# Kernel tuning notes

Hardware: AMD Instinct MI355X
Metric: run time of the kernel (lower is better)

## Reference

```python
import jax, jax.numpy as jnp
import numpy as np

HEADS = 8
DIM_HEAD = 32
SCALE = DIM_HEAD ** -0.5


def _split_heads(t):
    # [b, n, h*d] -> [b, h, n, d]
    b, n, hd = t.shape
    return t.reshape(b, n, HEADS, hd // HEADS).transpose(0, 2, 1, 3)


def setup_inputs() -> dict:
    key = jax.random.key(0)
    k1, k2, k3, k4 = jax.random.split(key, 4)
    b, n, dim = 2, 2048, 256
    inner = HEADS * DIM_HEAD  # 256
    x = jax.random.normal(k1, (b, n, dim), dtype=jnp.float32)
    attn_feat = jax.random.normal(k2, (b, n, dim), dtype=jnp.float32)
    # nn.Linear(dim, 3*inner, bias=False): store as [dim, 3*inner] for x @ W
    W_qkv = jax.random.normal(k3, (dim, 3 * inner), dtype=jnp.float32) * (dim ** -0.5)
    W_qkv_aux = jax.random.normal(k4, (dim, 3 * inner), dtype=jnp.float32) * (dim ** -0.5)
    return {"x": x, "attn_feat": attn_feat, "W_qkv": W_qkv, "W_qkv_aux": W_qkv_aux,
            "use_cls_tokens": 1}


def reference(x, attn_feat, W_qkv, W_qkv_aux, use_cls_tokens):
    b, n, dim = x.shape
    # aux Q,K (v_aux computed but unused, matching original chunk of 3)
    qkv_aux = attn_feat @ W_qkv_aux            # [b, n, 3*inner]
    q_aux, k_aux, _ = jnp.split(qkv_aux, 3, axis=-1)
    q_aux, k_aux = _split_heads(q_aux), _split_heads(k_aux)
    # self Q,K
    qkv_self = x @ W_qkv
    q_self, k_self, _ = jnp.split(qkv_self, 3, axis=-1)
    q_self, k_self = _split_heads(q_self), _split_heads(k_self)
    # dual score product: (QK^T_aux * scale) * (QK^T_self * scale)
    dots_aux = jnp.einsum('bhid,bhjd->bhij', q_aux, k_aux) * SCALE
    dots_self = jnp.einsum('bhid,bhjd->bhij', q_self, k_self) * SCALE
    attn = jax.nn.softmax(dots_aux * dots_self, axis=-1)  # [b, h, n, n]
    # v = x.unsqueeze(1): broadcast raw x over heads
    out = jnp.einsum('bhij,bjd->bhid', attn, x)           # [b, h, n, dim]
    out = out.transpose(0, 2, 1, 3).reshape(b, n, HEADS * dim)
    attn_flat = attn.transpose(0, 2, 1, 3).reshape(b, n, HEADS * n)
    return (out, out[:, 0], attn_flat[:, 0])
```

## Files before the change

### kernel.cpp

```cpp
#include <hip/hip_runtime.h>

typedef _Float16 f16;
typedef _Float16 f16x4 __attribute__((ext_vector_type(4)));
typedef _Float16 f16x8 __attribute__((ext_vector_type(8)));
typedef float f32x4 __attribute__((ext_vector_type(4)));

#define LOG2E 1.4426950408889634f
#define SCL   (1.4426950408889634f / 32.0f)
#define TH_RAW 177.445f

__global__ __launch_bounds__(256) void k_W(const float* __restrict__ Wq,
    const float* __restrict__ Wa, f16* __restrict__ Wt) {
  __shared__ f16 tile[64][65];
  int n0 = blockIdx.x * 64, k0 = blockIdx.y * 64, s = blockIdx.z;
  const float* W = s ? Wa : Wq;
  f16* dst = Wt + (size_t)s * 512 * 256;
  int t = threadIdx.x, c = t & 63, rg = t >> 6;
#pragma unroll
  for (int r = 0; r < 16; ++r) {
    int krow = r * 4 + rg;
    tile[krow][c] = (f16)W[(size_t)(k0 + krow) * 768 + n0 + c];
  }
  __syncthreads();
#pragma unroll
  for (int r = 0; r < 16; ++r) {
    int nrow = r * 4 + rg;
    dst[(size_t)(n0 + nrow) * 256 + k0 + c] = tile[c][nrow];
  }
}

__global__ __launch_bounds__(256) void k_proj(const float* __restrict__ x,
    const float* __restrict__ af, const f16* __restrict__ Wt,
    f16* __restrict__ Qs, f16* __restrict__ Ks,
    f16* __restrict__ Qa, f16* __restrict__ Ka, f16* __restrict__ xt) {
  __shared__ f16 tile[64][65];
  int t = threadIdx.x;
  if (blockIdx.x >= 64) {
    int r = ((blockIdx.z * 8 + blockIdx.y) * 16 + (blockIdx.x - 64));
    int n0 = (r & 31) * 64, d0 = ((r >> 5) & 3) * 64, b = r >> 7;
    int c = t & 63, rg = t >> 6;
#pragma unroll
    for (int rr = 0; rr < 16; ++rr) {
      int row = rr * 4 + rg;
      tile[row][c] = (f16)x[((size_t)b * 2048 + n0 + row) * 256 + d0 + c];
    }
    __syncthreads();
#pragma unroll
    for (int rr = 0; rr < 16; ++rr) {
      int drow = rr * 4 + rg;
      xt[((size_t)b * 256 + d0 + drow) * 2048 + n0 + c] = tile[c][drow];
    }
    return;
  }
  int mt = blockIdx.x, nt = blockIdx.y, s = blockIdx.z;
  const float* A = s ? af : x;
  const f16* W = Wt + (size_t)s * 512 * 256;
  f16* Qd = s ? Qa : Qs;
  f16* Kd = s ? Ka : Ks;
  int wv = t >> 6, ln = t & 63, cl = ln & 15, g = ln >> 4;
  int m0 = mt * 64, n0 = nt * 64;
  const float* arow = A + (size_t)(m0 + wv * 16 + cl) * 256 + g * 8;
  const f16* wb = W + (size_t)n0 * 256 + g * 8;
  f32x4 z4 = {0.f, 0.f, 0.f, 0.f};
  f32x4 acc[4] = {z4, z4, z4, z4};
#pragma unroll
  for (int k32 = 0; k32 < 8; ++k32) {
    float4 u = *(const float4*)(arow + k32 * 32);
    float4 v = *(const float4*)(arow + k32 * 32 + 4);
    f16x8 a = { (f16)u.x, (f16)u.y, (f16)u.z, (f16)u.w,
                (f16)v.x, (f16)v.y, (f16)v.z, (f16)v.w };
#pragma unroll
    for (int n4 = 0; n4 < 4; ++n4) {
      f16x8 bf = *(const f16x8*)(wb + (size_t)(n4 * 16 + cl) * 256 + k32 * 32);
      acc[n4] = __builtin_amdgcn_mfma_f32_16x16x32_f16(a, bf, acc[n4], 0, 0, 0);
    }
  }
#pragma unroll
  for (int n4 = 0; n4 < 4; ++n4) {
    int c = n0 + n4 * 16 + cl;
    int head = (c & 255) >> 5, d = c & 31;
    f16* dst = (c < 256) ? Qd : Kd;
#pragma unroll
    for (int r = 0; r < 4; ++r) {
      int m = m0 + wv * 16 + g * 4 + r;
      int bb = m >> 11, nn = m & 2047;
      dst[(((size_t)bb * 8 + head) * 2048 + nn) * 32 + d] = (f16)acc[n4][r];
    }
  }
}

__global__ __launch_bounds__(256, 2) void k_flash(const f16* __restrict__ Qs,
    const f16* __restrict__ Ks, const f16* __restrict__ Qa,
    const f16* __restrict__ Ka, const f16* __restrict__ xt,
    float* __restrict__ out, float* __restrict__ out_cls,
    float* __restrict__ attn0) {
  __shared__ f16 KaL[2][64][40];
  __shared__ f16 KsL[2][64][40];
  __shared__ f16 PL[2][64][72];
  __shared__ float alphaL[2][64] __attribute__((aligned(16)));
  __shared__ int   rsF[2][4] __attribute__((aligned(16)));
  __shared__ float lL[64];
  __shared__ float mHist[32];
  __shared__ float mFinS;
  int qt = blockIdx.x, h = blockIdx.y, b = blockIdx.z;
  int bh = b * 8 + h;
  int t = threadIdx.x, wv = t >> 6, ln = t & 63, cl = ln & 15, g = ln >> 4;
  bool isA0 = (qt == 0) && (wv == 0);
  float* a0base = attn0 + (size_t)b * 16384 + h * 2048;
  int qrow0 = qt * 64 + wv * 16;
  f16x8 qsf = *(const f16x8*)&Qs[((size_t)bh * 2048 + qrow0 + cl) * 32 + g * 8];
  f16x8 qaf = *(const f16x8*)&Qa[((size_t)bh * 2048 + qrow0 + cl) * 32 + g * 8];
  f32x4 z4 = {0.f, 0.f, 0.f, 0.f};
  f32x4 acc[4][4];
#pragma unroll
  for (int i = 0; i < 4; ++i)
#pragma unroll
    for (int j = 0; j < 4; ++j) acc[i][j] = z4;
  float m_run = -3.0e38f, l_lane = 0.f;
  int krow = t >> 2, koff = (t & 3) * 8;
  const f16* kaSrc = Ka + ((size_t)bh * 2048 + krow) * 32 + koff;
  const f16* ksSrc = Ks + ((size_t)bh * 2048 + krow) * 32 + koff;
  const f16* xb = xt + ((size_t)b * 256 + wv * 64) * 2048;

  float tv[16];
  f16x8 xf[2][4];

  auto SCORE_MM = [&](int buf) {
#pragma unroll
    for (int jt = 0; jt < 4; ++jt) {
      f16x8 kaf = *(const f16x8*)&KaL[buf][jt * 16 + cl][g * 8];
      f16x8 ksf = *(const f16x8*)&KsL[buf][jt * 16 + cl][g * 8];
      f32x4 za = __builtin_amdgcn_mfma_f32_16x16x32_f16(kaf, qaf, z4, 0, 0, 0);
      f32x4 zs = __builtin_amdgcn_mfma_f32_16x16x32_f16(ksf, qsf, z4, 0, 0, 0);
#pragma unroll
      for (int r = 0; r < 4; ++r) tv[jt * 4 + r] = za[r] * zs[r];
    }
  };

  auto SCORE_FIN = [&](int buf, int kt) {
    float a0 = fmaxf(tv[0], tv[1]),   a1 = fmaxf(tv[2], tv[3]);
    float a2 = fmaxf(tv[4], tv[5]),   a3 = fmaxf(tv[6], tv[7]);
    float a4 = fmaxf(tv[8], tv[9]),   a5 = fmaxf(tv[10], tv[11]);
    float a6 = fmaxf(tv[12], tv[13]), a7 = fmaxf(tv[14], tv[15]);
    float b0 = fmaxf(a0, a1), b1 = fmaxf(a2, a3);
    float b2 = fmaxf(a4, a5), b3 = fmaxf(a6, a7);
    float lmax = fmaxf(fmaxf(b0, b1), fmaxf(b2, b3));
    int wflag = 0;
    if (__any(lmax > m_run + TH_RAW)) {
      float tm = fmaxf(lmax, __shfl_xor(lmax, 16, 64));
      tm = fmaxf(tm, __shfl_xor(tm, 32, 64));
      float m_new = fmaxf(m_run, tm);
      float alpha = exp2f((m_run - m_new) * SCL);
      l_lane *= alpha;
      m_run = m_new;
      if (g == 0) alphaL[buf][wv * 16 + cl] = alpha;
      wflag = 1;
    }
    float mS = m_run * SCL;
    float p[16];
#pragma unroll
    for (int i = 0; i < 16; ++i) p[i] = exp2f(fmaf(tv[i], SCL, -mS));
    float s0 = p[0] + p[1],   s1 = p[2] + p[3];
    float s2 = p[4] + p[5],   s3 = p[6] + p[7];
    float s4 = p[8] + p[9],   s5 = p[10] + p[11];
    float s6 = p[12] + p[13], s7 = p[14] + p[15];
    float u0 = s0 + s1, u1 = s2 + s3, u2 = s4 + s5, u3 = s6 + s7;
    l_lane += (u0 + u1) + (u2 + u3);
#pragma unroll
    for (int jt = 0; jt < 4; ++jt) {
      auto lo = __builtin_amdgcn_cvt_pkrtz(p[jt * 4 + 0], p[jt * 4 + 1]);
      auto hi = __builtin_amdgcn_cvt_pkrtz(p[jt * 4 + 2], p[jt * 4 + 3]);
      f16x4 pk = { (f16)lo[0], (f16)lo[1], (f16)hi[0], (f16)hi[1] };
      *(f16x4*)&PL[buf][wv * 16 + cl][jt * 16 + g * 4] = pk;
    }
    if (ln == 0) rsF[buf][wv] = wflag;
    if (isA0) {
      if (ln == 0) mHist[kt] = m_run;
      if (cl == 0) {
#pragma unroll
        for (int jt = 0; jt < 4; ++jt) {
          float4 pw = { p[jt * 4 + 0], p[jt * 4 + 1],
                        p[jt * 4 + 2], p[jt * 4 + 3] };
          *(float4*)(a0base + kt * 64 + jt * 16 + g * 4) = pw;
        }
      }
    }
  };

  auto XFLOAD = [&](int kt) {
#pragma unroll
    for (int ks2 = 0; ks2 < 2; ++ks2)
#pragma unroll
      for (int ddt = 0; ddt < 4; ++ddt)
        xf[ks2][ddt] = *(const f16x8*)(xb + (size_t)(ddt * 16 + cl) * 2048 +
                                       kt * 64 + ks2 * 32 + g * 8);
  };

  auto PVDO = [&](int pbuf) {
    int4 fl = *(const int4*)&rsF[pbuf][0];
    int flq[4] = { fl.x, fl.y, fl.z, fl.w };
#pragma unroll
    for (int qt2 = 0; qt2 < 4; ++qt2) {
      if (flq[qt2]) {
        f32x4 a4 = *(const f32x4*)&alphaL[pbuf][qt2 * 16 + g * 4];
#pragma unroll
        for (int ddt = 0; ddt < 4; ++ddt)
#pragma unroll
          for (int r = 0; r < 4; ++r) acc[qt2][ddt][r] *= a4[r];
      }
    }
#pragma unroll
    for (int ks2 = 0; ks2 < 2; ++ks2) {
      f16x8 pf[4];
#pragma unroll
      for (int qt2 = 0; qt2 < 4; ++qt2)
        pf[qt2] = *(const f16x8*)&PL[pbuf][qt2 * 16 + cl][ks2 * 32 + g * 8];
#pragma unroll
      for (int ddt = 0; ddt < 4; ++ddt)
#pragma unroll
        for (int qt2 = 0; qt2 < 4; ++qt2)
          acc[qt2][ddt] = __builtin_amdgcn_mfma_f32_16x16x32_f16(
              pf[qt2], xf[ks2][ddt], acc[qt2][ddt], 0, 0, 0);
    }
  };

  *(f16x8*)&KaL[0][krow][koff] = *(const f16x8*)kaSrc;
  *(f16x8*)&KsL[0][krow][koff] = *(const f16x8*)ksSrc;
  __syncthreads();

  f16x8 kan = *(const f16x8*)(kaSrc + 2048);
  f16x8 ksn = *(const f16x8*)(ksSrc + 2048);
  SCORE_MM(0);
  SCORE_FIN(0, 0);
  *(f16x8*)&KaL[1][krow][koff] = kan;
  *(f16x8*)&KsL[1][krow][koff] = ksn;
  __syncthreads();

  for (int k = 1; k < 32; ++k) {
    int sbuf = k & 1, pbuf = sbuf ^ 1;
    XFLOAD(k - 1);
    if (k < 31) {
      kan = *(const f16x8*)(kaSrc + (size_t)(k + 1) * 2048);
      ksn = *(const f16x8*)(ksSrc + (size_t)(k + 1) * 2048);
    }
    SCORE_MM(sbuf);
    PVDO(pbuf);
    SCORE_FIN(sbuf, k);
    if (k < 31) {
      *(f16x8*)&KaL[pbuf][krow][koff] = kan;
      *(f16x8*)&KsL[pbuf][krow][koff] = ksn;
    }
    __syncthreads();
  }

  XFLOAD(31);
  PVDO(1);

  l_lane += __shfl_xor(l_lane, 16, 64);
  l_lane += __shfl_xor(l_lane, 32, 64);
  if (g == 0) lL[wv * 16 + cl] = l_lane;
  if (isA0 && ln == 0) mFinS = m_run;
  __syncthreads();
#pragma unroll
  for (int qt2 = 0; qt2 < 4; ++qt2) {
#pragma unroll
    for (int r = 0; r < 4; ++r) {
      float linv = 1.0f / lL[qt2 * 16 + g * 4 + r];
      int q = qt * 64 + qt2 * 16 + g * 4 + r;
#pragma unroll
      for (int ddt = 0; ddt < 4; ++ddt) {
        float v = acc[qt2][ddt][r] * linv;
        int col = h * 256 + wv * 64 + ddt * 16 + cl;
        out[((size_t)b * 2048 + q) * 2048 + col] = v;
        if (q == 0) out_cls[(size_t)b * 2048 + col] = v;
      }
    }
  }
  if (qt == 0) {
    float l0inv = 1.0f / lL[0];
    float mf = mFinS;
    for (int i = t; i < 2048; i += 256) {
      float v = a0base[i];
      a0base[i] = v * exp2f((mHist[i >> 6] - mf) * SCL) * l0inv;
    }
  }
}

extern "C" void kernel_launch(void* const* d_in, const int* in_sizes, int n_in,
                              void* d_out, int out_size, void* d_ws, size_t ws_size,
                              hipStream_t stream) {
  const float* x  = (const float*)d_in[0];
  const float* af = (const float*)d_in[1];
  const float* Wq = (const float*)d_in[2];
  const float* Wa = (const float*)d_in[3];
  const size_t QK = (size_t)2 * 8 * 2048 * 32;
  f16* Qs = (f16*)d_ws;
  f16* Ks = Qs + QK;
  f16* Qa = Ks + QK;
  f16* Ka = Qa + QK;
  f16* xt = Ka + QK;
  f16* Wt = xt + QK;
  float* out     = (float*)d_out;
  float* out_cls = out + (size_t)2 * 2048 * 2048;
  float* attn0   = out_cls + 2 * 2048;

  k_W<<<dim3(8, 4, 2), 256, 0, stream>>>(Wq, Wa, Wt);
  k_proj<<<dim3(80, 8, 2), 256, 0, stream>>>(x, af, Wt, Qs, Ks, Qa, Ka, xt);
  k_flash<<<dim3(32, 8, 2), 256, 0, stream>>>(Qs, Ks, Qa, Ka, xt, out, out_cls,
                                              attn0);
}
```

Before: 174.5 us.

## Move x transpose into weight-staging kernel and reuse A rows across all N tiles

```diff
diff --git a/kernel.cpp b/kernel.cpp
--- a/kernel.cpp
+++ b/kernel.cpp
@@ -9,82 +9,88 @@
 #define SCL   (1.4426950408889634f / 32.0f)
 #define TH_RAW 177.445f
 
-__global__ __launch_bounds__(256) void k_W(const float* __restrict__ Wq,
-    const float* __restrict__ Wa, f16* __restrict__ Wt) {
+__global__ __launch_bounds__(256) void k_stage(const float* __restrict__ x,
+    const float* __restrict__ Wq, const float* __restrict__ Wa,
+    f16* __restrict__ xt, f16* __restrict__ Wt) {
   __shared__ f16 tile[64][65];
-  int n0 = blockIdx.x * 64, k0 = blockIdx.y * 64, s = blockIdx.z;
-  const float* W = s ? Wa : Wq;
-  f16* dst = Wt + (size_t)s * 512 * 256;
   int t = threadIdx.x, c = t & 63, rg = t >> 6;
-#pragma unroll
-  for (int r = 0; r < 16; ++r) {
-    int krow = r * 4 + rg;
-    tile[krow][c] = (f16)W[(size_t)(k0 + krow) * 768 + n0 + c];
-  }
-  __syncthreads();
-#pragma unroll
-  for (int r = 0; r < 16; ++r) {
-    int nrow = r * 4 + rg;
-    dst[(size_t)(n0 + nrow) * 256 + k0 + c] = tile[c][nrow];
+  if (blockIdx.x < 32) {
+    int n0 = blockIdx.x * 64, d0 = blockIdx.y * 64, b = blockIdx.z;
+#pragma unroll
+    for (int r = 0; r < 16; ++r) {
+      int row = r * 4 + rg;
+      tile[row][c] = (f16)x[((size_t)b * 2048 + n0 + row) * 256 + d0 + c];
+    }
+    __syncthreads();
+#pragma unroll
+    for (int r = 0; r < 16; ++r) {
+      int drow = r * 4 + rg;
+      xt[((size_t)b * 256 + d0 + drow) * 2048 + n0 + c] = tile[c][drow];
+    }
+  } else {
+    int n0 = (blockIdx.x - 32) * 64, k0 = blockIdx.y * 64, s = blockIdx.z;
+    const float* W = s ? Wa : Wq;
+    f16* dst = Wt + (size_t)s * 512 * 256;
+#pragma unroll
+    for (int r = 0; r < 16; ++r) {
+      int krow = r * 4 + rg;
+      tile[krow][c] = (f16)W[(size_t)(k0 + krow) * 768 + n0 + c];
+    }
+    __syncthreads();
+#pragma unroll
+    for (int r = 0; r < 16; ++r) {
+      int nrow = r * 4 + rg;
+      dst[(size_t)(n0 + nrow) * 256 + k0 + c] = tile[c][nrow];
+    }
   }
 }
 
 __global__ __launch_bounds__(256) void k_proj(const float* __restrict__ x,
     const float* __restrict__ af, const f16* __restrict__ Wt,
     f16* __restrict__ Qs, f16* __restrict__ Ks,
-    f16* __restrict__ Qa, f16* __restrict__ Ka, f16* __restrict__ xt) {
-  __shared__ f16 tile[64][65];
-  int t = threadIdx.x;
-  if (blockIdx.x >= 64) {
-    int r = ((blockIdx.z * 8 + blockIdx.y) * 16 + (blockIdx.x - 64));
-    int n0 = (r & 31) * 64, d0 = ((r >> 5) & 3) * 64, b = r >> 7;
-    int c = t & 63, rg = t >> 6;
-#pragma unroll
-    for (int rr = 0; rr < 16; ++rr) {
-      int row = rr * 4 + rg;
-      tile[row][c] = (f16)x[((size_t)b * 2048 + n0 + row) * 256 + d0 + c];
-    }
-    __syncthreads();
-#pragma unroll
-    for (int rr = 0; rr < 16; ++rr) {
-      int drow = rr * 4 + rg;
-      xt[((size_t)b * 256 + d0 + drow) * 2048 + n0 + c] = tile[c][drow];
-    }
-    return;
-  }
-  int mt = blockIdx.x, nt = blockIdx.y, s = blockIdx.z;
+    f16* __restrict__ Qa, f16* __restrict__ Ka) {
+  int mt = blockIdx.x, s = blockIdx.y;
   const float* A = s ? af : x;
-  const f16* W = Wt + (size_t)s * 512 * 256;
+  const f16* Wb = Wt + (size_t)s * 512 * 256;
   f16* Qd = s ? Qa : Qs;
   f16* Kd = s ? Ka : Ks;
-  int wv = t >> 6, ln = t & 63, cl = ln & 15, g = ln >> 4;
-  int m0 = mt * 64, n0 = nt * 64;
+  int t = threadIdx.x, wv = t >> 6, ln = t & 63, cl = ln & 15, g = ln >> 4;
+  int m0 = mt * 64;
   const float* arow = A + (size_t)(m0 + wv * 16 + cl) * 256 + g * 8;
-  const f16* wb = W + (size_t)n0 * 256 + g * 8;
-  f32x4 z4 = {0.f, 0.f, 0.f, 0.f};
-  f32x4 acc[4] = {z4, z4, z4, z4};
+  f16x8 areg[8];
 #pragma unroll
   for (int k32 = 0; k32 < 8; ++k32) {
     float4 u = *(const float4*)(arow + k32 * 32);
     float4 v = *(const float4*)(arow + k32 * 32 + 4);
-    f16x8 a = { (f16)u.x, (f16)u.y, (f16)u.z, (f16)u.w,
-                (f16)v.x, (f16)v.y, (f16)v.z, (f16)v.w };
+    areg[k32] = (f16x8){ (f16)u.x, (f16)u.y, (f16)u.z, (f16)u.w,
+                         (f16)v.x, (f16)v.y, (f16)v.z, (f16)v.w };
+  }
+  f32x4 z4 = {0.f, 0.f, 0.f, 0.f};
+#pragma unroll
+  for (int nt = 0; nt < 8; ++nt) {
+    int n0 = nt * 64;
+    const f16* wb = Wb + (size_t)n0 * 256 + g * 8;
+    f32x4 acc[4] = {z4, z4, z4, z4};
+#pragma unroll
+    for (int k32 = 0; k32 < 8; ++k32) {
+#pragma unroll
+      for (int n4 = 0; n4 < 4; ++n4) {
+        f16x8 bf = *(const f16x8*)(wb + (size_t)(n4 * 16 + cl) * 256 + k32 * 32);
+        acc[n4] = __builtin_amdgcn_mfma_f32_16x16x32_f16(areg[k32], bf, acc[n4],
+                                                         0, 0, 0);
+      }
+    }
 #pragma unroll
     for (int n4 = 0; n4 < 4; ++n4) {
-      f16x8 bf = *(const f16x8*)(wb + (size_t)(n4 * 16 + cl) * 256 + k32 * 32);
-      acc[n4] = __builtin_amdgcn_mfma_f32_16x16x32_f16(a, bf, acc[n4], 0, 0, 0);
-    }
-  }
-#pragma unroll
-  for (int n4 = 0; n4 < 4; ++n4) {
-    int c = n0 + n4 * 16 + cl;
-    int head = (c & 255) >> 5, d = c & 31;
-    f16* dst = (c < 256) ? Qd : Kd;
-#pragma unroll
-    for (int r = 0; r < 4; ++r) {
-      int m = m0 + wv * 16 + g * 4 + r;
-      int bb = m >> 11, nn = m & 2047;
-      dst[(((size_t)bb * 8 + head) * 2048 + nn) * 32 + d] = (f16)acc[n4][r];
+      int c = n0 + n4 * 16 + cl;
+      int head = (c & 255) >> 5, d = c & 31;
+      f16* dst = (c < 256) ? Qd : Kd;
+#pragma unroll
+      for (int r = 0; r < 4; ++r) {
+        int m = m0 + wv * 16 + g * 4 + r;
+        int bb = m >> 11, nn = m & 2047;
+        dst[(((size_t)bb * 8 + head) * 2048 + nn) * 32 + d] = (f16)acc[n4][r];
+      }
     }
   }
 }
@@ -304,8 +310,8 @@
   float* out_cls = out + (size_t)2 * 2048 * 2048;
   float* attn0   = out_cls + 2 * 2048;
 
-  k_W<<<dim3(8, 4, 2), 256, 0, stream>>>(Wq, Wa, Wt);
-  k_proj<<<dim3(80, 8, 2), 256, 0, stream>>>(x, af, Wt, Qs, Ks, Qa, Ka, xt);
+  k_stage<<<dim3(40, 4, 2), 256, 0, stream>>>(x, Wq, Wa, xt, Wt);
+  k_proj<<<dim3(64, 2), 256, 0, stream>>>(x, af, Wt, Qs, Ks, Qa, Ka);
   k_flash<<<dim3(32, 8, 2), 256, 0, stream>>>(Qs, Ks, Qa, Ka, xt, out, out_cls,
                                               attn0);
 }
```

Measured after the change: 202.3 us. 15.9% more time.
